# Kernel optimization log

Measured on AMD Instinct MI355X. Metric: run time of the kernel, lower is better.

## Reference

```python
import jax, jax.numpy as jnp
import numpy as np

N_NODES = 50000
N_EDGES = 600000
N_GRAPHS = 64
D_IN = 128
D_HID = 128
D_LAT = 64
BN_EPS = 1e-5


def setup_inputs() -> dict:
    key = jax.random.key(0)
    ks = jax.random.split(key, 8)
    x = jax.random.normal(ks[0], (N_NODES, D_IN), dtype=jnp.float32)
    edge_index = jax.random.randint(ks[1], (2, N_EDGES), 0, N_NODES, dtype=jnp.int64 if jax.config.jax_enable_x64 else jnp.int32)
    batch = jnp.sort(jax.random.randint(ks[2], (N_NODES,), 0, N_GRAPHS))
    d_cat = 13 * D_IN  # x + (mean,max,min,std) x (identity,amp,att)
    s = 1.0 / np.sqrt(d_cat)
    W0 = jax.random.normal(ks[3], (d_cat, D_HID), dtype=jnp.float32) * s
    W1 = jax.random.normal(ks[4], (13 * D_HID, D_HID), dtype=jnp.float32) * s
    W2 = jax.random.normal(ks[5], (13 * D_HID, D_HID), dtype=jnp.float32) * s
    fcW = jax.random.normal(ks[6], (D_HID, D_LAT), dtype=jnp.float32) * (1.0 / np.sqrt(D_HID))
    return {
        "x": x, "edge_index": edge_index, "batch": batch,
        "W0": W0, "b0": jnp.zeros((D_HID,), jnp.float32),
        "W1": W1, "b1": jnp.zeros((D_HID,), jnp.float32),
        "W2": W2, "b2": jnp.zeros((D_HID,), jnp.float32),
        "bn_gamma": jnp.ones((D_HID,), jnp.float32),
        "bn_beta": jnp.zeros((D_HID,), jnp.float32),
        "fcW": fcW, "fcb": jnp.zeros((D_LAT,), jnp.float32),
    }


def _pna_conv(h, W, b, src, dst, deg, delta):
    # h: [N, d]; messages gathered from source nodes per edge: [E, d]
    m = h[src]
    cnt = jnp.maximum(deg, 1.0)[:, None]
    ssum = jax.ops.segment_sum(m, dst, num_segments=N_NODES)
    mean = ssum / cnt
    ssq = jax.ops.segment_sum(m * m, dst, num_segments=N_NODES)
    std = jnp.sqrt(jnp.maximum(ssq / cnt - mean * mean, 0.0) + 1e-5)
    mx = jax.ops.segment_max(m, dst, num_segments=N_NODES)
    mn = jax.ops.segment_min(m, dst, num_segments=N_NODES)
    has = (deg > 0)[:, None]
    mx = jnp.where(has, mx, 0.0)
    mn = jnp.where(has, mn, 0.0)
    agg = jnp.concatenate([mean, mx, mn, std], axis=-1)  # [N, 4d]
    logd = jnp.log(deg + 1.0)[:, None]
    amp = logd / delta
    att = delta / jnp.maximum(logd, 1e-5)
    feat = jnp.concatenate([h, agg, agg * amp, agg * att], axis=-1)  # [N, 13d]
    return feat @ W + b


def reference(x, edge_index, batch, W0, b0, W1, b1, W2, b2, bn_gamma, bn_beta, fcW, fcb):
    src, dst = edge_index[0], edge_index[1]
    deg = jax.ops.segment_sum(jnp.ones((src.shape[0],), x.dtype), dst, num_segments=N_NODES)
    delta = jnp.mean(jnp.log(deg + 1.0))  # avg log-degree normalizer
    h = jax.nn.relu(_pna_conv(x, W0, b0, src, dst, deg, delta))
    h = jax.nn.relu(_pna_conv(h, W1, b1, src, dst, deg, delta))
    h = jax.nn.relu(_pna_conv(h, W2, b2, src, dst, deg, delta))
    # dropout is identity in eval mode
    pooled = jax.ops.segment_sum(h, batch, num_segments=N_GRAPHS)  # global_add_pool
    mu = jnp.mean(pooled, axis=0)
    var = jnp.var(pooled, axis=0)
    bn = (pooled - mu) / jnp.sqrt(var + BN_EPS) * bn_gamma + bn_beta
    return bn @ fcW + fcb
```

## Files before the change

### kernel.cpp

```cpp
#include <hip/hip_runtime.h>
#include <cstdint>
#include <cstddef>

#define N_NODESC 50000
#define N_PAD    50048
#define N_EDGESC 600000
#define N_GRAPHSC 64
#define D_HIDC   128
#define D_LATC   64
#define D_G      640
#define D_WROW   1664

typedef unsigned short u16;
typedef unsigned int   u32;

typedef _Float16 f16x8 __attribute__((ext_vector_type(8)));
typedef _Float16 f16x2 __attribute__((ext_vector_type(2)));
typedef float    f32x4 __attribute__((ext_vector_type(4)));
typedef float    f32x2 __attribute__((ext_vector_type(2)));

__device__ __forceinline__ u16 f2h(float f) {
    return __builtin_bit_cast(u16, (_Float16)f);
}
__device__ __forceinline__ float h2f(u16 u) {
    return (float)__builtin_bit_cast(_Float16, u);
}

__device__ __forceinline__ void gll16(void* lds, const void* g) {
    __builtin_amdgcn_global_load_lds(
        (const __attribute__((address_space(1))) void*)g,
        (__attribute__((address_space(3))) void*)lds, 16, 0, 0);
}

__global__ void __launch_bounds__(256) k_setup(
        const float* __restrict__ x, const float* __restrict__ W0,
        const float* __restrict__ W1, const float* __restrict__ W2,
        const int* __restrict__ batch,
        u16* __restrict__ h, u16* __restrict__ Wt,
        int* __restrict__ zero_base, int nz, int ZB, int* __restrict__ goff) {
    int b = blockIdx.x;
    int t = threadIdx.x;
    if (b < ZB) {
        int i = b * 256 + t;
        if (i < nz) zero_base[i] = 0;
        return;
    }
    b -= ZB;
    if (b < 12500) {
        int i = b * 256 + t;
        float2 v = ((const float2*)x)[i];
        ((u32*)h)[i] = (u32)f2h(v.x) | ((u32)f2h(v.y) << 16);
        return;
    }
    b -= 12500;
    if (b < 2496) {
        int which = b / 832;
        int i = (b % 832) * 256 + t;
        const float* W = (which == 0) ? W0 : (which == 1) ? W1 : W2;
        int k = i / D_HIDC, j = i % D_HIDC;
        Wt[(size_t)which * D_WROW * D_HIDC + (size_t)j * D_WROW + k] = f2h(W[i]);
        return;
    }
    int g = t;
    if (g <= N_GRAPHSC) {
        int lo = 0, hi = N_NODESC;
        while (lo < hi) {
            int mid = (lo + hi) >> 1;
            if (batch[mid] < g) lo = mid + 1; else hi = mid;
        }
        goff[g] = lo;
    }
}

__global__ void k_count(const int* __restrict__ dst, int* __restrict__ deg) {
    int e = blockIdx.x * 256 + threadIdx.x;
    if (e < N_EDGESC) atomicAdd(&deg[dst[e]], 1);
}

__global__ void __launch_bounds__(256) k_scan_part(
        const int* __restrict__ deg, int* __restrict__ bsum,
        float* __restrict__ lsum) {
    __shared__ int s[256];
    __shared__ float ls[256];
    int idx = blockIdx.x * 256 + threadIdx.x;
    int v = (idx < N_NODESC) ? deg[idx] : 0;
    s[threadIdx.x] = v;
    ls[threadIdx.x] = (idx < N_NODESC) ? logf((float)v + 1.0f) : 0.0f;
    __syncthreads();
    for (int o = 128; o > 0; o >>= 1) {
        if (threadIdx.x < o) {
            s[threadIdx.x] += s[threadIdx.x + o];
            ls[threadIdx.x] += ls[threadIdx.x + o];
        }
        __syncthreads();
    }
    if (threadIdx.x == 0) { bsum[blockIdx.x] = s[0]; lsum[blockIdx.x] = ls[0]; }
}

__global__ void __launch_bounds__(256) k_scan_block(
        int* __restrict__ bsum, const float* __restrict__ lsum,
        float* __restrict__ delta_p) {
    __shared__ int s[256];
    __shared__ float ls[256];
    int t = threadIdx.x;
    int v = (t < 196) ? bsum[t] : 0;
    s[t] = v;
    ls[t] = (t < 196) ? lsum[t] : 0.0f;
    __syncthreads();
    for (int o = 1; o < 256; o <<= 1) {
        int add = (t >= o) ? s[t - o] : 0;
        __syncthreads();
        s[t] += add;
        __syncthreads();
    }
    if (t < 196) bsum[t] = s[t] - v;
    for (int o = 128; o > 0; o >>= 1) {
        if (t < o) ls[t] += ls[t + o];
        __syncthreads();
    }
    if (t == 0) delta_p[0] = ls[0] * (1.0f / (float)N_NODESC);
}

__global__ void __launch_bounds__(256) k_scan_final(
        const int* __restrict__ deg, const int* __restrict__ bsum,
        int* __restrict__ row_off) {
    __shared__ int s[256];
    int t = threadIdx.x;
    int idx = blockIdx.x * 256 + t;
    int v = (idx < N_NODESC) ? deg[idx] : 0;
    s[t] = v; __syncthreads();
    for (int o = 1; o < 256; o <<= 1) {
        int add = (t >= o) ? s[t - o] : 0;
        __syncthreads();
        s[t] += add;
        __syncthreads();
    }
    int excl = s[t] - v + bsum[blockIdx.x];
    if (idx < N_NODESC) row_off[idx] = excl;
    if (idx == 0) row_off[N_NODESC] = N_EDGESC;
}

__global__ void k_fill_csr(const int* __restrict__ src, const int* __restrict__ dst,
                           const int* __restrict__ row_off, int* __restrict__ cursor,
                           int* __restrict__ csr_src) {
    int e = blockIdx.x * 256 + threadIdx.x;
    if (e < N_EDGESC) {
        int d = dst[e];
        int pos = row_off[d] + atomicAdd(&cursor[d], 1);
        csr_src[pos] = src[e];
    }
}


__global__ void __launch_bounds__(256) k_aggregate(
        const u16* __restrict__ h, const int* __restrict__ row_off,
        const int* __restrict__ csr_src, u16* __restrict__ G) {
    int n = blockIdx.x * 4 + (threadIdx.x >> 6);
    if (n >= N_NODESC) return;
    int lane = threadIdx.x & 63;
    int half = lane >> 5, l32 = lane & 31;
    int c4 = 4 * l32;
    int beg = row_off[n], end = row_off[n + 1];
    const _Float16 NEG = (_Float16)(-65504.0f), POS = (_Float16)(65504.0f);
    f32x2 s01 = {0.f, 0.f}, s23 = {0.f, 0.f};
    f32x2 q01 = {0.f, 0.f}, q23 = {0.f, 0.f};
    f16x2 mx01 = {NEG, NEG}, mx23 = {NEG, NEG};
    f16x2 mn01 = {POS, POS}, mn23 = {POS, POS};

    #define PROC(u) { \
        f16x2 p01 = __builtin_bit_cast(f16x2, (u).x); \
        f16x2 p23 = __builtin_bit_cast(f16x2, (u).y); \
        f32x2 c01 = __builtin_convertvector(p01, f32x2); \
        f32x2 c23 = __builtin_convertvector(p23, f32x2); \
        s01 += c01; s23 += c23; \
        q01 += c01 * c01; q23 += c23 * c23; \
        mx01 = __builtin_elementwise_max(mx01, p01); \
        mx23 = __builtin_elementwise_max(mx23, p23); \
        mn01 = __builtin_elementwise_min(mn01, p01); \
        mn23 = __builtin_elementwise_min(mn23, p23); }

    int i = beg + half;
    for (; i + 6 < end; i += 8) {
        int e0 = csr_src[i],     e1 = csr_src[i + 2];
        int e2 = csr_src[i + 4], e3 = csr_src[i + 6];
        uint2 u0 = *(const uint2*)(h + (size_t)e0 * D_HIDC + c4);
        uint2 u1 = *(const uint2*)(h + (size_t)e1 * D_HIDC + c4);
        uint2 u2 = *(const uint2*)(h + (size_t)e2 * D_HIDC + c4);
        uint2 u3 = *(const uint2*)(h + (size_t)e3 * D_HIDC + c4);
        PROC(u0); PROC(u1); PROC(u2); PROC(u3);
    }
    for (; i < end; i += 2) {
        int e0 = csr_src[i];
        uint2 u0 = *(const uint2*)(h + (size_t)e0 * D_HIDC + c4);
        PROC(u0);
    }
    #undef PROC

    s01.x += __shfl_xor(s01.x, 32); s01.y += __shfl_xor(s01.y, 32);
    s23.x += __shfl_xor(s23.x, 32); s23.y += __shfl_xor(s23.y, 32);
    q01.x += __shfl_xor(q01.x, 32); q01.y += __shfl_xor(q01.y, 32);
    q23.x += __shfl_xor(q23.x, 32); q23.y += __shfl_xor(q23.y, 32);
    #define MRG(v, OP) v = OP(v, \
        __builtin_bit_cast(f16x2, __shfl_xor(__builtin_bit_cast(int, v), 32)))
    MRG(mx01, __builtin_elementwise_max); MRG(mx23, __builtin_elementwise_max);
    MRG(mn01, __builtin_elementwise_min); MRG(mn23, __builtin_elementwise_min);
    #undef MRG

    int d = end - beg;
    float inv = 1.0f / fmaxf((float)d, 1.0f);
    float me0 = s01.x * inv, me1 = s01.y * inv;
    float me2 = s23.x * inv, me3 = s23.y * inv;
    float sd0 = sqrtf(fmaxf(q01.x * inv - me0 * me0, 0.0f) + 1e-5f);
    float sd1 = sqrtf(fmaxf(q01.y * inv - me1 * me1, 0.0f) + 1e-5f);
    float sd2 = sqrtf(fmaxf(q23.x * inv - me2 * me2, 0.0f) + 1e-5f);
    float sd3 = sqrtf(fmaxf(q23.y * inv - me3 * me3, 0.0f) + 1e-5f);
    float fx0 = (float)mx01.x, fx1 = (float)mx01.y;
    float fx2 = (float)mx23.x, fx3 = (float)mx23.y;
    float fn0 = (float)mn01.x, fn1 = (float)mn01.y;
    float fn2 = (float)mn23.x, fn3 = (float)mn23.y;
    if (d == 0) {
        fx0 = fx1 = fx2 = fx3 = 0.0f;
        fn0 = fn1 = fn2 = fn3 = 0.0f;
    }
    u16* base = G + (size_t)n * D_G;
    #define PK2(a, b) ((u32)f2h(a) | ((u32)f2h(b) << 16))
    if (half == 0) {
        *(uint2*)(base + c4) = *(const uint2*)(h + (size_t)n * D_HIDC + c4);
        uint2 m; m.x = PK2(me0, me1); m.y = PK2(me2, me3);
        *(uint2*)(base + 128 + c4) = m;
        uint2 X; X.x = PK2(fx0, fx1); X.y = PK2(fx2, fx3);
        *(uint2*)(base + 256 + c4) = X;
    } else {
        uint2 N_; N_.x = PK2(fn0, fn1); N_.y = PK2(fn2, fn3);
        *(uint2*)(base + 384 + c4) = N_;
        uint2 S; S.x = PK2(sd0, sd1); S.y = PK2(sd2, sd3);
        *(uint2*)(base + 512 + c4) = S;
    }
    #undef PK2
}

__global__ void __launch_bounds__(256) k_gemm(
        const u16* __restrict__ G, const u16* __restrict__ Wt,
        const int* __restrict__ deg, const float* __restrict__ delta_p,
        const float* __restrict__ bias, u16* __restrict__ hout) {
    __shared__ _Float16 A1[128 * 64];
    __shared__ _Float16 A2[128 * 64];
    __shared__ _Float16 A3[128 * 64];
    __shared__ _Float16 Bt[64 * 64];
    const _Float16* Wf = (const _Float16*)Wt;
    const _Float16* Gf = (const _Float16*)G;
    int n0 = blockIdx.x * 64;
    int t = threadIdx.x;
    int w = t >> 6, lane = t & 63;
    int srow8 = lane >> 3, sslot = lane & 7;
    int stg = (sslot ^ srow8) * 8;
    int q4 = lane >> 4, r16 = lane & 15;
    int sx0 = (q4 ^ (lane & 7)) * 8;
    int sx1 = ((q4 + 4) ^ (lane & 7)) * 8;
    int col = lane & 15;

    float delta = delta_p[0];
    float atv[4];
    _Float16 amh[4];
    #pragma unroll
    for (int nt = 0; nt < 4; nt++) {
        int node = n0 + nt * 16 + col;
        float logd = logf((float)deg[node] + 1.0f);
        amh[nt] = (_Float16)(logd / delta);
        atv[nt] = delta / fmaxf(logd, 1e-5f);
    }

    f32x4 acc[2][4], ac3[2][4];
    #pragma unroll
    for (int a = 0; a < 2; a++)
        #pragma unroll
        for (int b = 0; b < 4; b++) {
            acc[a][b] = (f32x4){0.f, 0.f, 0.f, 0.f};
            ac3[a][b] = (f32x4){0.f, 0.f, 0.f, 0.f};
        }

    for (int ki = 0; ki < 10; ki++) {
        int k0 = ki * 64;
        bool sreg = (k0 >= 128);
        __syncthreads();
        #pragma unroll
        for (int r = 0; r < 4; r++) {
            int rr = r * 4 + w;
            const _Float16* wrow = Wf + (size_t)(rr * 8 + srow8) * D_WROW;
            gll16(&A1[rr * 512], wrow + k0 + stg);
        }
        if (sreg) {
            #pragma unroll
            for (int r = 0; r < 4; r++) {
                int rr = r * 4 + w;
                const _Float16* wrow = Wf + (size_t)(rr * 8 + srow8) * D_WROW;
                gll16(&A2[rr * 512], wrow + 512 + k0 + stg);
                gll16(&A3[rr * 512], wrow + 1024 + k0 + stg);
            }
        }
        #pragma unroll
        for (int q = 0; q < 2; q++) {
            int rr = q * 4 + w;
            gll16(&Bt[rr * 512], Gf + (size_t)(n0 + rr * 8 + srow8) * D_G + k0 + stg);
        }
        __syncthreads();
        f16x8 a00 = *(const f16x8*)&A1[(w * 32 + r16) * 64 + sx0];
        f16x8 a01 = *(const f16x8*)&A1[(w * 32 + r16) * 64 + sx1];
        f16x8 a10 = *(const f16x8*)&A1[(w * 32 + 16 + r16) * 64 + sx0];
        f16x8 a11 = *(const f16x8*)&A1[(w * 32 + 16 + r16) * 64 + sx1];
        if (!sreg) {
            #pragma unroll
            for (int nt = 0; nt < 4; nt++) {
                f16x8 b0 = *(const f16x8*)&Bt[(nt * 16 + r16) * 64 + sx0];
                f16x8 b1 = *(const f16x8*)&Bt[(nt * 16 + r16) * 64 + sx1];
                acc[0][nt] = __builtin_amdgcn_mfma_f32_16x16x32_f16(a00, b0, acc[0][nt], 0, 0, 0);
                acc[1][nt] = __builtin_amdgcn_mfma_f32_16x16x32_f16(a10, b0, acc[1][nt], 0, 0, 0);
                acc[0][nt] = __builtin_amdgcn_mfma_f32_16x16x32_f16(a01, b1, acc[0][nt], 0, 0, 0);
                acc[1][nt] = __builtin_amdgcn_mfma_f32_16x16x32_f16(a11, b1, acc[1][nt], 0, 0, 0);
            }
        } else {
            f16x8 w2a0 = *(const f16x8*)&A2[(w * 32 + r16) * 64 + sx0];
            f16x8 w2a1 = *(const f16x8*)&A2[(w * 32 + r16) * 64 + sx1];
            f16x8 w2b0 = *(const f16x8*)&A2[(w * 32 + 16 + r16) * 64 + sx0];
            f16x8 w2b1 = *(const f16x8*)&A2[(w * 32 + 16 + r16) * 64 + sx1];
            f16x8 w3a0 = *(const f16x8*)&A3[(w * 32 + r16) * 64 + sx0];
            f16x8 w3a1 = *(const f16x8*)&A3[(w * 32 + r16) * 64 + sx1];
            f16x8 w3b0 = *(const f16x8*)&A3[(w * 32 + 16 + r16) * 64 + sx0];
            f16x8 w3b1 = *(const f16x8*)&A3[(w * 32 + 16 + r16) * 64 + sx1];
            #pragma unroll
            for (int nt = 0; nt < 4; nt++) {
                f16x8 b0 = *(const f16x8*)&Bt[(nt * 16 + r16) * 64 + sx0];
                f16x8 b1 = *(const f16x8*)&Bt[(nt * 16 + r16) * 64 + sx1];
                f16x8 bm0 = b0 * amh[nt];
                f16x8 bm1 = b1 * amh[nt];
                acc[0][nt] = __builtin_amdgcn_mfma_f32_16x16x32_f16(a00, b0, acc[0][nt], 0, 0, 0);
                acc[1][nt] = __builtin_amdgcn_mfma_f32_16x16x32_f16(a10, b0, acc[1][nt], 0, 0, 0);
                acc[0][nt] = __builtin_amdgcn_mfma_f32_16x16x32_f16(a01, b1, acc[0][nt], 0, 0, 0);
                acc[1][nt] = __builtin_amdgcn_mfma_f32_16x16x32_f16(a11, b1, acc[1][nt], 0, 0, 0);
                acc[0][nt] = __builtin_amdgcn_mfma_f32_16x16x32_f16(w2a0, bm0, acc[0][nt], 0, 0, 0);
                acc[1][nt] = __builtin_amdgcn_mfma_f32_16x16x32_f16(w2b0, bm0, acc[1][nt], 0, 0, 0);
                acc[0][nt] = __builtin_amdgcn_mfma_f32_16x16x32_f16(w2a1, bm1, acc[0][nt], 0, 0, 0);
                acc[1][nt] = __builtin_amdgcn_mfma_f32_16x16x32_f16(w2b1, bm1, acc[1][nt], 0, 0, 0);
                ac3[0][nt] = __builtin_amdgcn_mfma_f32_16x16x32_f16(w3a0, b0, ac3[0][nt], 0, 0, 0);
                ac3[1][nt] = __builtin_amdgcn_mfma_f32_16x16x32_f16(w3b0, b0, ac3[1][nt], 0, 0, 0);
                ac3[0][nt] = __builtin_amdgcn_mfma_f32_16x16x32_f16(w3a1, b1, ac3[0][nt], 0, 0, 0);
                ac3[1][nt] = __builtin_amdgcn_mfma_f32_16x16x32_f16(w3b1, b1, ac3[1][nt], 0, 0, 0);
            }
        }
    }
    int rowq = q4 * 4;
    #pragma unroll
    for (int nt = 0; nt < 4; nt++) {
        int node = n0 + nt * 16 + col;
        float at = atv[nt];
        #pragma unroll
        for (int mt = 0; mt < 2; mt++) {
            int jb = w * 32 + mt * 16 + rowq;
            f32x4 v = acc[mt][nt], v3 = ac3[mt][nt];
            ushort4 o;
            o.x = f2h(fmaxf(v.x + at * v3.x + bias[jb], 0.0f));
            o.y = f2h(fmaxf(v.y + at * v3.y + bias[jb + 1], 0.0f));
            o.z = f2h(fmaxf(v.z + at * v3.z + bias[jb + 2], 0.0f));
            o.w = f2h(fmaxf(v.w + at * v3.w + bias[jb + 3], 0.0f));
            *(ushort4*)&hout[(size_t)node * D_HIDC + jb] = o;
        }
    }
}


__global__ void __launch_bounds__(256) k_pool(
        const u16* __restrict__ h, const int* __restrict__ goff,
        float* __restrict__ pooled) {
    __shared__ float sm[256];
    int g = blockIdx.x >> 2, s = blockIdx.x & 3;
    int gb = goff[g], ge = goff[g + 1];
    int len = ge - gb;
    int q = (len + 3) >> 2;
    int nb = gb + s * q;
    int ne = min(nb + q, ge);
    int t = threadIdx.x;
    int j = t & 127, half = t >> 7;
    float acc = 0.0f;
    for (int n = nb + half; n < ne; n += 2)
        acc += h2f(h[(size_t)n * D_HIDC + j]);
    sm[t] = acc; __syncthreads();
    if (t < 128) {
        float v = sm[t] + sm[t + 128];
        atomicAdd(&pooled[g * D_HIDC + j], v);
    }
}

__global__ void __launch_bounds__(128) k_bn_fc(
        const float* __restrict__ pooled, const float* __restrict__ gamma,
        const float* __restrict__ beta, const float* __restrict__ fcW,
        const float* __restrict__ fcb, float* __restrict__ out) {
    __shared__ float bn[D_HIDC];
    int g = blockIdx.x, t = threadIdx.x;
    float s = 0.f, q = 0.f;
    for (int gg = 0; gg < N_GRAPHSC; gg++) {
        float v = pooled[gg * D_HIDC + t];
        s += v; q += v * v;
    }
    float mu = s * (1.0f / N_GRAPHSC);
    float var = q * (1.0f / N_GRAPHSC) - mu * mu;
    float inv = 1.0f / sqrtf(var + 1e-5f);
    bn[t] = (pooled[g * D_HIDC + t] - mu) * inv * gamma[t] + beta[t];
    __syncthreads();
    if (t < D_LATC) {
        float accum = fcb[t];
        for (int j = 0; j < D_HIDC; j++) accum += bn[j] * fcW[j * D_LATC + t];
        out[g * D_LATC + t] = accum;
    }
}


extern "C" void kernel_launch(void* const* d_in, const int* in_sizes, int n_in,
                              void* d_out, int out_size, void* d_ws, size_t ws_size,
                              hipStream_t stream) {
    const float* x     = (const float*)d_in[0];
    const int*   ei    = (const int*)d_in[1];
    const int*   batch = (const int*)d_in[2];
    const float* W0 = (const float*)d_in[3];
    const float* b0 = (const float*)d_in[4];
    const float* W1 = (const float*)d_in[5];
    const float* b1 = (const float*)d_in[6];
    const float* W2 = (const float*)d_in[7];
    const float* b2 = (const float*)d_in[8];
    const float* gamma = (const float*)d_in[9];
    const float* beta  = (const float*)d_in[10];
    const float* fcW   = (const float*)d_in[11];
    const float* fcb   = (const float*)d_in[12];
    float* out = (float*)d_out;
    const int* srcv = ei;
    const int* dstv = ei + N_EDGESC;

    char* p = (char*)d_ws;
    auto alloc = [&](size_t bytes) -> char* {
        char* r = p;
        p += (bytes + 255) & ~(size_t)255;
        return r;
    };
    int*   deg_cnt = (int*)alloc((size_t)N_PAD * 4);
    int*   cursor  = (int*)alloc((size_t)N_NODESC * 4);
    float* delta_p = (float*)alloc(4);
    float* pooled  = (float*)alloc((size_t)N_GRAPHSC * D_HIDC * 4);
    char*  zero_end = p;
    int*   row_off = (int*)alloc((size_t)(N_NODESC + 1) * 4);
    int*   goff    = (int*)alloc((size_t)(N_GRAPHSC + 1) * 4);
    int*   bsum    = (int*)alloc(256 * 4);
    float* lsum    = (float*)alloc(256 * 4);
    int*   csr_src = (int*)alloc((size_t)N_EDGESC * 4);
    u16*   Wt      = (u16*)alloc((size_t)3 * D_WROW * D_HIDC * 2);
    u16*   hA      = (u16*)alloc((size_t)N_PAD * D_HIDC * 2);
    u16*   hB      = (u16*)alloc((size_t)N_PAD * D_HIDC * 2);
    u16*   G       = (u16*)alloc((size_t)N_PAD * D_G * 2);

    int nz = (int)((zero_end - (char*)deg_cnt) / 4);
    int ZB = (nz + 255) / 256;
    int setup_grid = ZB + 12500 + 2496 + 1;
    k_setup<<<setup_grid, 256, 0, stream>>>(x, W0, W1, W2, batch,
                                            hB, Wt, deg_cnt, nz, ZB, goff);
    k_count<<<(N_EDGESC + 255) / 256, 256, 0, stream>>>(dstv, deg_cnt);
    k_scan_part<<<196, 256, 0, stream>>>(deg_cnt, bsum, lsum);
    k_scan_block<<<1, 256, 0, stream>>>(bsum, lsum, delta_p);
    k_scan_final<<<196, 256, 0, stream>>>(deg_cnt, bsum, row_off);
    k_fill_csr<<<(N_EDGESC + 255) / 256, 256, 0, stream>>>(srcv, dstv, row_off, cursor, csr_src);

    const float* bs[3] = {b0, b1, b2};
    const u16* h_in[3]  = {hB, hA, hB};
    u16*       h_out[3] = {hA, hB, hA};
    size_t wsz = (size_t)D_WROW * D_HIDC;
    for (int l = 0; l < 3; l++) {
        k_aggregate<<<(N_NODESC + 3) / 4, 256, 0, stream>>>(
            h_in[l], row_off, csr_src, G);
        k_gemm<<<N_PAD / 64, 256, 0, stream>>>(
            G, Wt + (size_t)l * wsz, deg_cnt, delta_p, bs[l], h_out[l]);
    }
    k_pool<<<4 * N_GRAPHSC, 256, 0, stream>>>(h_out[2], goff, pooled);
    k_bn_fc<<<N_GRAPHSC, 128, 0, stream>>>(pooled, gamma, beta, fcW, fcb, out);
}
```

Before: 422.4 us.

## Load GEMM weights directly into registers and double-buffer node feature tiles

The GEMM kernel no longer stages weight tiles through shared memory. Each lane reads its MFMA A-operand fragments straight from global memory (L2-resident weights). The node-feature B tile is double-buffered in LDS, so the next K-slice is prefetched while the current one is consumed, with one barrier per iteration instead of two. LDS use drops from about 56KB to 16KB, and launch bounds request three blocks per CU to raise occupancy, at the cost of more global load traffic and register pressure.

```diff
diff --git a/kernel.cpp b/kernel.cpp
--- a/kernel.cpp
+++ b/kernel.cpp
@@ -239,14 +239,11 @@
     #undef PK2
 }
 
-__global__ void __launch_bounds__(256) k_gemm(
+__global__ void __launch_bounds__(256, 3) k_gemm(
         const u16* __restrict__ G, const u16* __restrict__ Wt,
         const int* __restrict__ deg, const float* __restrict__ delta_p,
         const float* __restrict__ bias, u16* __restrict__ hout) {
-    __shared__ _Float16 A1[128 * 64];
-    __shared__ _Float16 A2[128 * 64];
-    __shared__ _Float16 A3[128 * 64];
-    __shared__ _Float16 Bt[64 * 64];
+    __shared__ _Float16 Bt[2][64 * 64];
     const _Float16* Wf = (const _Float16*)Wt;
     const _Float16* Gf = (const _Float16*)G;
     int n0 = blockIdx.x * 64;
@@ -259,6 +256,9 @@
     int sx1 = ((q4 + 4) ^ (lane & 7)) * 8;
     int col = lane & 15;
 
+    const _Float16* pW0 = Wf + (size_t)(w * 32 + r16) * D_WROW + q4 * 8;
+    const _Float16* pW1 = pW0 + (size_t)16 * D_WROW;
+
     float delta = delta_p[0];
     float atv[4];
     _Float16 amh[4];
@@ -279,58 +279,55 @@
             ac3[a][b] = (f32x4){0.f, 0.f, 0.f, 0.f};
         }
 
+    #pragma unroll
+    for (int q = 0; q < 2; q++) {
+        int rr = q * 4 + w;
+        gll16(&Bt[0][rr * 512], Gf + (size_t)(n0 + rr * 8 + srow8) * D_G + stg);
+    }
+    __syncthreads();
+
+    int cur = 0;
+    #pragma unroll
     for (int ki = 0; ki < 10; ki++) {
         int k0 = ki * 64;
         bool sreg = (k0 >= 128);
-        __syncthreads();
-        #pragma unroll
-        for (int r = 0; r < 4; r++) {
-            int rr = r * 4 + w;
-            const _Float16* wrow = Wf + (size_t)(rr * 8 + srow8) * D_WROW;
-            gll16(&A1[rr * 512], wrow + k0 + stg);
-        }
-        if (sreg) {
+        if (ki < 9) {
+            int k1 = k0 + 64;
             #pragma unroll
-            for (int r = 0; r < 4; r++) {
-                int rr = r * 4 + w;
-                const _Float16* wrow = Wf + (size_t)(rr * 8 + srow8) * D_WROW;
-                gll16(&A2[rr * 512], wrow + 512 + k0 + stg);
-                gll16(&A3[rr * 512], wrow + 1024 + k0 + stg);
+            for (int q = 0; q < 2; q++) {
+                int rr = q * 4 + w;
+                gll16(&Bt[cur ^ 1][rr * 512],
+                      Gf + (size_t)(n0 + rr * 8 + srow8) * D_G + k1 + stg);
             }
         }
-        #pragma unroll
-        for (int q = 0; q < 2; q++) {
-            int rr = q * 4 + w;
-            gll16(&Bt[rr * 512], Gf + (size_t)(n0 + rr * 8 + srow8) * D_G + k0 + stg);
-        }
-        __syncthreads();
-        f16x8 a00 = *(const f16x8*)&A1[(w * 32 + r16) * 64 + sx0];
-        f16x8 a01 = *(const f16x8*)&A1[(w * 32 + r16) * 64 + sx1];
-        f16x8 a10 = *(const f16x8*)&A1[(w * 32 + 16 + r16) * 64 + sx0];
-        f16x8 a11 = *(const f16x8*)&A1[(w * 32 + 16 + r16) * 64 + sx1];
+        const _Float16* bb = Bt[cur];
+        f16x8 a00 = *(const f16x8*)(pW0 + k0);
+        f16x8 a01 = *(const f16x8*)(pW0 + k0 + 32);
+        f16x8 a10 = *(const f16x8*)(pW1 + k0);
+        f16x8 a11 = *(const f16x8*)(pW1 + k0 + 32);
         if (!sreg) {
             #pragma unroll
             for (int nt = 0; nt < 4; nt++) {
-                f16x8 b0 = *(const f16x8*)&Bt[(nt * 16 + r16) * 64 + sx0];
-                f16x8 b1 = *(const f16x8*)&Bt[(nt * 16 + r16) * 64 + sx1];
+                f16x8 b0 = *(const f16x8*)&bb[(nt * 16 + r16) * 64 + sx0];
+                f16x8 b1 = *(const f16x8*)&bb[(nt * 16 + r16) * 64 + sx1];
                 acc[0][nt] = __builtin_amdgcn_mfma_f32_16x16x32_f16(a00, b0, acc[0][nt], 0, 0, 0);
                 acc[1][nt] = __builtin_amdgcn_mfma_f32_16x16x32_f16(a10, b0, acc[1][nt], 0, 0, 0);
                 acc[0][nt] = __builtin_amdgcn_mfma_f32_16x16x32_f16(a01, b1, acc[0][nt], 0, 0, 0);
                 acc[1][nt] = __builtin_amdgcn_mfma_f32_16x16x32_f16(a11, b1, acc[1][nt], 0, 0, 0);
             }
         } else {
-            f16x8 w2a0 = *(const f16x8*)&A2[(w * 32 + r16) * 64 + sx0];
-            f16x8 w2a1 = *(const f16x8*)&A2[(w * 32 + r16) * 64 + sx1];
-            f16x8 w2b0 = *(const f16x8*)&A2[(w * 32 + 16 + r16) * 64 + sx0];
-            f16x8 w2b1 = *(const f16x8*)&A2[(w * 32 + 16 + r16) * 64 + sx1];
-            f16x8 w3a0 = *(const f16x8*)&A3[(w * 32 + r16) * 64 + sx0];
-            f16x8 w3a1 = *(const f16x8*)&A3[(w * 32 + r16) * 64 + sx1];
-            f16x8 w3b0 = *(const f16x8*)&A3[(w * 32 + 16 + r16) * 64 + sx0];
-            f16x8 w3b1 = *(const f16x8*)&A3[(w * 32 + 16 + r16) * 64 + sx1];
+            f16x8 w2a0 = *(const f16x8*)(pW0 + 512 + k0);
+            f16x8 w2a1 = *(const f16x8*)(pW0 + 512 + k0 + 32);
+            f16x8 w2b0 = *(const f16x8*)(pW1 + 512 + k0);
+            f16x8 w2b1 = *(const f16x8*)(pW1 + 512 + k0 + 32);
+            f16x8 w3a0 = *(const f16x8*)(pW0 + 1024 + k0);
+            f16x8 w3a1 = *(const f16x8*)(pW0 + 1024 + k0 + 32);
+            f16x8 w3b0 = *(const f16x8*)(pW1 + 1024 + k0);
+            f16x8 w3b1 = *(const f16x8*)(pW1 + 1024 + k0 + 32);
             #pragma unroll
             for (int nt = 0; nt < 4; nt++) {
-                f16x8 b0 = *(const f16x8*)&Bt[(nt * 16 + r16) * 64 + sx0];
-                f16x8 b1 = *(const f16x8*)&Bt[(nt * 16 + r16) * 64 + sx1];
+                f16x8 b0 = *(const f16x8*)&bb[(nt * 16 + r16) * 64 + sx0];
+                f16x8 b1 = *(const f16x8*)&bb[(nt * 16 + r16) * 64 + sx1];
                 f16x8 bm0 = b0 * amh[nt];
                 f16x8 bm1 = b1 * amh[nt];
                 acc[0][nt] = __builtin_amdgcn_mfma_f32_16x16x32_f16(a00, b0, acc[0][nt], 0, 0, 0);
@@ -347,6 +344,8 @@
                 ac3[1][nt] = __builtin_amdgcn_mfma_f32_16x16x32_f16(w3b1, b1, ac3[1][nt], 0, 0, 0);
             }
         }
+        __syncthreads();
+        cur ^= 1;
     }
     int rowq = q4 * 4;
     #pragma unroll
```

Measured after the change: 503.7 us. 19.2% more time.
